# Optimization experiments

Measured on AMD Instinct MI355X. Metric: run time of the kernel, lower is better.

Reference implementation:

```python
import jax, jax.numpy as jnp
import numpy as np

B, IMG, PATCH = 32, 224, 16
D_MODEL, DEPTH = 384, 24
D_INNER, D_STATE, DT_RANK, D_CONV = 768, 16, 24, 4
L = (IMG // PATCH) ** 2  # 196 patch tokens
NCLS = 1000
EPS = 1e-5


def _layernorm(x, w, b):
    mu = x.mean(-1, keepdims=True)
    var = ((x - mu) ** 2).mean(-1, keepdims=True)
    return (x - mu) * jax.lax.rsqrt(var + EPS) * w + b


def _mamba(x, p):
    # x: [B, L, D_MODEL] -> Mamba mixer (expand=2, d_state=16, d_conv=4)
    xz = jnp.einsum('bld,ed->ble', x, p['W_in'])  # [B,L,2*di]
    xc, z = jnp.split(xz, 2, axis=-1)
    # depthwise causal conv over the sequence dim
    xt = jnp.moveaxis(xc, 1, 2)  # [B,di,L]
    xt = jnp.pad(xt, ((0, 0), (0, 0), (D_CONV - 1, 0)))
    xt = jax.lax.conv_general_dilated(xt, p['conv_w'][:, None, :], (1,), 'VALID',
                                      dimension_numbers=('NCH', 'OIH', 'NCH'),
                                      feature_group_count=D_INNER)
    xc = jax.nn.silu(jnp.moveaxis(xt, 1, 2) + p['conv_b'])  # [B,L,di]
    proj = jnp.einsum('ble,re->blr', xc, p['W_xp'])  # [B,L,dt_rank+2*ns]
    dt, Bs, Cs = jnp.split(proj, [DT_RANK, DT_RANK + D_STATE], axis=-1)
    delta = jax.nn.softplus(jnp.einsum('blr,er->ble', dt, p['W_dt']) + p['b_dt'])  # [B,L,di]
    A = -jnp.exp(p['A_log'])  # [di, ns]

    def step(h, inputs):
        # compute discretization per-step: avoids materializing [B,L,di,ns]
        d_t, B_t, C_t, u_t = inputs  # [B,di],[B,ns],[B,ns],[B,di]
        h = jnp.exp(d_t[:, :, None] * A) * h + (d_t * u_t)[:, :, None] * B_t[:, None, :]
        return h, jnp.einsum('bdn,bn->bd', h, C_t)

    h0 = jnp.zeros((x.shape[0], D_INNER, D_STATE), x.dtype)
    seq = (jnp.moveaxis(delta, 1, 0), jnp.moveaxis(Bs, 1, 0),
           jnp.moveaxis(Cs, 1, 0), jnp.moveaxis(xc, 1, 0))
    _, ys = jax.lax.scan(step, h0, seq)
    y = jnp.moveaxis(ys, 0, 1) + xc * p['D_p']
    y = y * jax.nn.silu(z)
    return jnp.einsum('ble,de->bld', y, p['W_out'])


def _forward(x, patch_w, patch_b, pos_embed, W_in, conv_w, conv_b, W_xp, W_dt,
             b_dt, A_log, D_p, W_out, ln_w, ln_b, normf_w, normf_b, head_w, head_b):
    # patch embed: conv stride 16, flatten to tokens
    h = jax.lax.conv_general_dilated(x, patch_w, (PATCH, PATCH), 'VALID',
                                     dimension_numbers=('NCHW', 'OIHW', 'NCHW'))
    h = h + patch_b[None, :, None, None]
    h = h.reshape(x.shape[0], D_MODEL, L).transpose(0, 2, 1)  # [B,L,D]
    h = h + pos_embed
    params = dict(W_in=W_in, conv_w=conv_w, conv_b=conv_b, W_xp=W_xp, W_dt=W_dt,
                  b_dt=b_dt, A_log=A_log, D_p=D_p, W_out=W_out, ln_w=ln_w, ln_b=ln_b)

    def block(carry, p):
        # Block: Add -> LN -> Mamba, carrying (hidden, residual)
        hidden, residual = carry
        residual = residual + hidden
        hidden = _mamba(_layernorm(residual, p['ln_w'], p['ln_b']), p)
        return (hidden, residual), None

    (hidden, residual), _ = jax.lax.scan(block, (h, jnp.zeros_like(h)), params)
    residual = residual + hidden
    h = _layernorm(residual, normf_w, normf_b)
    pooled = h.mean(axis=1)  # final_pool_type='mean'
    return pooled @ head_w.T + head_b


def setup_inputs():
    key = jax.random.key(0)
    ks = jax.random.split(key, 12)

    def rn(k, shape, scale=0.02):
        return jax.random.normal(k, shape, jnp.float32) * scale

    inp = {}
    inp['x'] = jax.random.normal(ks[0], (B, 3, IMG, IMG), jnp.float32)
    inp['patch_w'] = rn(ks[1], (D_MODEL, 3, PATCH, PATCH), 0.05)
    inp['patch_b'] = jnp.zeros((D_MODEL,), jnp.float32)
    inp['pos_embed'] = rn(ks[2], (1, L, D_MODEL))
    inp['W_in'] = rn(ks[3], (DEPTH, 2 * D_INNER, D_MODEL))
    inp['conv_w'] = rn(ks[4], (DEPTH, D_INNER, D_CONV), 0.1)
    inp['conv_b'] = jnp.zeros((DEPTH, D_INNER), jnp.float32)
    inp['W_xp'] = rn(ks[5], (DEPTH, DT_RANK + 2 * D_STATE, D_INNER))
    inp['W_dt'] = rn(ks[6], (DEPTH, D_INNER, DT_RANK), 0.1)
    inp['b_dt'] = jnp.full((DEPTH, D_INNER), -4.6, jnp.float32) + rn(ks[7], (DEPTH, D_INNER), 0.1)
    Ainit = jnp.tile(jnp.arange(1, D_STATE + 1, dtype=jnp.float32)[None, None, :], (DEPTH, D_INNER, 1))
    inp['A_log'] = jnp.log(Ainit)  # S4D-real init
    inp['D_p'] = jnp.ones((DEPTH, D_INNER), jnp.float32)
    inp['W_out'] = rn(ks[8], (DEPTH, D_MODEL, D_INNER))
    inp['ln_w'] = jnp.ones((DEPTH, D_MODEL), jnp.float32)
    inp['ln_b'] = jnp.zeros((DEPTH, D_MODEL), jnp.float32)
    inp['normf_w'] = jnp.ones((D_MODEL,), jnp.float32)
    inp['normf_b'] = jnp.zeros((D_MODEL,), jnp.float32)
    inp['head_w'] = rn(ks[9], (NCLS, D_MODEL))
    inp['head_b'] = jnp.zeros((NCLS,), jnp.float32)
    return inp


def reference(x, patch_w, patch_b, pos_embed, W_in, conv_w, conv_b, W_xp, W_dt,
              b_dt, A_log, D_p, W_out, ln_w, ln_b, normf_w, normf_b, head_w, head_b):
    return _forward(x, patch_w, patch_b, pos_embed, W_in, conv_w, conv_b, W_xp,
                    W_dt, b_dt, A_log, D_p, W_out, ln_w, ln_b, normf_w, normf_b,
                    head_w, head_b)
```

## Files before the change

kernel.cpp:

```cpp
#include <hip/hip_runtime.h>
#include <hip/hip_bf16.h>
#include <math.h>

#define BB      32
#define LTOK    196
#define DMODEL  384
#define DINNER  768
#define DSTATE  16
#define DTRANK  24
#define DCONV   4
#define PROJW   64
#define NTOK    (BB*LTOK)
#define NCLS    1000
#define EPS     1e-5f

typedef __attribute__((ext_vector_type(8))) short short8v;
typedef __attribute__((ext_vector_type(4))) float f32x4;

static __device__ __forceinline__ ushort f2bf(float f) {
    unsigned u = __float_as_uint(f);
    unsigned r = (u + 0x7fffu + ((u >> 16) & 1u)) >> 16;
    return (ushort)r;
}
static __device__ __forceinline__ float bf2f(ushort h) {
    return __uint_as_float(((unsigned)h) << 16);
}

__global__ void cast_bf16_kernel(const float* __restrict__ src,
                                 ushort* __restrict__ dst, int n4)
{
    int stride = gridDim.x * blockDim.x;
    for (int i = blockIdx.x * blockDim.x + threadIdx.x; i < n4; i += stride) {
        float4 v = ((const float4*)src)[i];
        ushort4 o;
        o.x = f2bf(v.x); o.y = f2bf(v.y); o.z = f2bf(v.z); o.w = f2bf(v.w);
        ((ushort4*)dst)[i] = o;
    }
}

__global__ void pad_wxp_kernel(const float* __restrict__ src, ushort* __restrict__ dst)
{
    int idx = blockIdx.x * 256 + threadIdx.x;
    if (idx >= 24 * 64 * 768) return;
    int c = idx % 768;
    int r = (idx / 768) & 63;
    int l = idx / (64 * 768);
    dst[idx] = (r < 56) ? f2bf(src[((size_t)l * 56 + r) * 768 + c]) : (ushort)0;
}

__global__ void pad_wdt_kernel(const float* __restrict__ src, ushort* __restrict__ dst)
{
    int idx = blockIdx.x * 256 + threadIdx.x;
    if (idx >= 24 * 768 * 32) return;
    int c = idx & 31;
    int r = (idx / 32) % 768;
    int l = idx / (768 * 32);
    dst[idx] = (c < 24) ? f2bf(src[((size_t)l * 768 + r) * 24 + c]) : (ushort)0;
}

template<int BM, int BN>
__global__ __launch_bounds__(256) void gemm_mfma(
    const ushort* __restrict__ A,
    const ushort* __restrict__ B,
    float* __restrict__ Cf, ushort* __restrict__ Cbf,
    int N, int K,
    const float* __restrict__ bias,
    const float* __restrict__ rowbias,
    int act, int mode)
{
    constexpr int MI = BM / 32;
    constexpr int NI = BN / 32;
    __shared__ __align__(16) ushort As[BM * 40];
    __shared__ __align__(16) ushort Bs[BN * 40];
    const int t    = threadIdx.x;
    const int lane = t & 63;
    const int wave = t >> 6;
    const int wr   = wave >> 1;
    const int wc   = wave & 1;
    const int lr   = lane & 15;
    const int lk   = lane >> 4;
    const int bm   = blockIdx.x * BM;
    const int bn   = blockIdx.y * BN;

    f32x4 acc[MI][NI];
    #pragma unroll
    for (int i = 0; i < MI; i++)
        #pragma unroll
        for (int j = 0; j < NI; j++) acc[i][j] = (f32x4){0.f, 0.f, 0.f, 0.f};

    for (int k0 = 0; k0 < K; k0 += 32) {
        #pragma unroll
        for (int i = 0; i < BM / 64; i++) {
            int c = t + i * 256;
            int row = c >> 2, kc = (c & 3) * 8;
            *(int4*)&As[row * 40 + kc] = *(const int4*)&A[(size_t)(bm + row) * K + k0 + kc];
        }
        #pragma unroll
        for (int i = 0; i < BN / 64; i++) {
            int c = t + i * 256;
            int row = c >> 2, kc = (c & 3) * 8;
            *(int4*)&Bs[row * 40 + kc] = *(const int4*)&B[(size_t)(bn + row) * K + k0 + kc];
        }
        __syncthreads();
        short8v af[MI], bfr[NI];
        #pragma unroll
        for (int mi = 0; mi < MI; mi++)
            af[mi] = *(short8v*)&As[(wr * (BM / 2) + mi * 16 + lr) * 40 + lk * 8];
        #pragma unroll
        for (int ni = 0; ni < NI; ni++)
            bfr[ni] = *(short8v*)&Bs[(wc * (BN / 2) + ni * 16 + lr) * 40 + lk * 8];
        #pragma unroll
        for (int mi = 0; mi < MI; mi++)
            #pragma unroll
            for (int ni = 0; ni < NI; ni++)
                acc[mi][ni] = __builtin_amdgcn_mfma_f32_16x16x32_bf16(
                    af[mi], bfr[ni], acc[mi][ni], 0, 0, 0);
        __syncthreads();
    }

    #pragma unroll
    for (int mi = 0; mi < MI; mi++) {
        #pragma unroll
        for (int ni = 0; ni < NI; ni++) {
            int col = bn + wc * (BN / 2) + ni * 16 + lr;
            float bv = bias ? bias[col] : 0.f;
            #pragma unroll
            for (int j = 0; j < 4; j++) {
                int row = bm + wr * (BM / 2) + mi * 16 + lk * 4 + j;
                float v = acc[mi][ni][j] + bv;
                if (rowbias) v += rowbias[(size_t)(row % LTOK) * N + col];
                if (act == 1) v = (v > 20.f) ? v : logf(1.f + __expf(v));
                if (mode == 0) {
                    Cf[(size_t)row * N + col] = v;
                } else if (mode == 1) {
                    Cbf[(size_t)row * N + col] = f2bf(v);
                } else {
                    Cf[(size_t)row * N + col] = v;
                    if (col < 32)
                        Cbf[(size_t)row * 32 + col] = (col < DTRANK) ? f2bf(v) : (ushort)0;
                }
            }
        }
    }
}

__global__ void im2col_kernel(const float* __restrict__ x, ushort* __restrict__ col)
{
    int idx = blockIdx.x * 256 + threadIdx.x;
    if (idx >= NTOK * 768) return;
    int k = idx % 768;
    int m = idx / 768;
    int b = m / LTOK, l = m % LTOK;
    int ph = l / 14, pw = l % 14;
    int c = k / 256, rr = k % 256;
    int i = rr / 16, j = rr % 16;
    col[idx] = f2bf(x[(((size_t)b * 3 + c) * 224 + ph * 16 + i) * 224 + pw * 16 + j]);
}

__global__ __launch_bounds__(64) void add_ln_kernel(
    float* __restrict__ residual, const float* __restrict__ hidden,
    const float* __restrict__ w, const float* __restrict__ b,
    float* __restrict__ xln, ushort* __restrict__ xln_bf)
{
    const int token = blockIdx.x;
    const int lane  = threadIdx.x;
    const size_t base = (size_t)token * DMODEL;
    float v[6];
    float sum = 0.f;
    #pragma unroll
    for (int i = 0; i < 6; i++) {
        int d = lane + i * 64;
        float r = residual[base + d] + hidden[base + d];
        v[i] = r;
        sum += r;
    }
    #pragma unroll
    for (int off = 32; off > 0; off >>= 1) sum += __shfl_xor(sum, off);
    float mu = sum * (1.f / DMODEL);
    float var = 0.f;
    #pragma unroll
    for (int i = 0; i < 6; i++) { float c = v[i] - mu; var += c * c; }
    #pragma unroll
    for (int off = 32; off > 0; off >>= 1) var += __shfl_xor(var, off);
    var *= (1.f / DMODEL);
    float rstd = rsqrtf(var + EPS);
    #pragma unroll
    for (int i = 0; i < 6; i++) {
        int d = lane + i * 64;
        residual[base + d] = v[i];
        float o = (v[i] - mu) * rstd * w[d] + b[d];
        xln[base + d]    = o;
        xln_bf[base + d] = f2bf(o);
    }
}

__global__ __launch_bounds__(256) void conv_silu_kernel(
    const ushort* __restrict__ xz,
    const float* __restrict__ cw,
    const float* __restrict__ cb,
    float* __restrict__ out,
    ushort* __restrict__ out_bf)
{
    int idx = blockIdx.x * 256 + threadIdx.x;
    if (idx >= NTOK * DINNER) return;
    int e = idx % DINNER;
    int m = idx / DINNER;
    int b = m / LTOK, tpos = m % LTOK;
    float4 w4 = ((const float4*)cw)[e];
    float wv[4] = {w4.x, w4.y, w4.z, w4.w};
    float acc = cb[e];
    #pragma unroll
    for (int tau = 0; tau < DCONV; tau++) {
        int l = tpos - (DCONV - 1) + tau;
        if (l >= 0)
            acc += wv[tau] * bf2f(xz[((size_t)(b * LTOK + l)) * (2 * DINNER) + e]);
    }
    float s = acc / (1.f + __expf(-acc));
    out[idx]    = s;
    out_bf[idx] = f2bf(s);
}

__global__ __launch_bounds__(64) void scan_kernel(
    const float* __restrict__ delta,
    const float* __restrict__ u,
    const float* __restrict__ proj,
    const ushort* __restrict__ xz,
    const float* __restrict__ A_log,
    const float* __restrict__ Dp,
    ushort* __restrict__ y)
{
    const int b = blockIdx.x;
    const int d = blockIdx.y * 64 + threadIdx.x;
    float Arow[DSTATE];
    #pragma unroll
    for (int n = 0; n < DSTATE; n++) Arow[n] = -__expf(A_log[(size_t)d * DSTATE + n]);
    const float ddp = Dp[d];
    float h[DSTATE];
    #pragma unroll
    for (int n = 0; n < DSTATE; n++) h[n] = 0.f;

    for (int l = 0; l < LTOK; l++) {
        const size_t row = (size_t)b * LTOK + l;
        const float dt = delta[row * DINNER + d];
        const float ut = u[row * DINNER + d];
        float Bv[DSTATE], Cv[DSTATE];
        const float4* prB = (const float4*)(proj + row * PROJW + DTRANK);
        const float4* prC = (const float4*)(proj + row * PROJW + DTRANK + DSTATE);
        #pragma unroll
        for (int q = 0; q < 4; q++) {
            float4 b4 = prB[q];
            Bv[q*4+0]=b4.x; Bv[q*4+1]=b4.y; Bv[q*4+2]=b4.z; Bv[q*4+3]=b4.w;
            float4 c4 = prC[q];
            Cv[q*4+0]=c4.x; Cv[q*4+1]=c4.y; Cv[q*4+2]=c4.z; Cv[q*4+3]=c4.w;
        }
        const float du = dt * ut;
        float acc = 0.f;
        #pragma unroll
        for (int n = 0; n < DSTATE; n++) {
            h[n] = __expf(dt * Arow[n]) * h[n] + du * Bv[n];
            acc += h[n] * Cv[n];
        }
        float zz = bf2f(xz[row * (2 * DINNER) + DINNER + d]);
        float g  = zz / (1.f + __expf(-zz));
        y[row * DINNER + d] = f2bf((acc + ut * ddp) * g);
    }
}

__global__ __launch_bounds__(256) void pool_kernel(const float* __restrict__ xln,
                                                   float* __restrict__ pooled)
{
    int idx = blockIdx.x * 256 + threadIdx.x;
    if (idx >= BB * DMODEL) return;
    int b = idx / DMODEL, d = idx % DMODEL;
    float s = 0.f;
    for (int l = 0; l < LTOK; l++) s += xln[((size_t)b * LTOK + l) * DMODEL + d];
    pooled[idx] = s * (1.f / LTOK);
}

__global__ __launch_bounds__(256) void head_kernel(const float* __restrict__ pooled,
                                                   const float* __restrict__ hw,
                                                   const float* __restrict__ hb,
                                                   float* __restrict__ out)
{
    int idx = blockIdx.x * 256 + threadIdx.x;
    if (idx >= BB * NCLS) return;
    int b = idx / NCLS, n = idx % NCLS;
    float s = hb[n];
    const float* p = pooled + (size_t)b * DMODEL;
    const float* w = hw + (size_t)n * DMODEL;
    for (int k = 0; k < DMODEL; k++) s += p[k] * w[k];
    out[idx] = s;
}

extern "C" void kernel_launch(void* const* d_in, const int* in_sizes, int n_in,
                              void* d_out, int out_size, void* d_ws, size_t ws_size,
                              hipStream_t stream)
{
    const float* x       = (const float*)d_in[0];
    const float* patch_w = (const float*)d_in[1];
    const float* patch_b = (const float*)d_in[2];
    const float* pos     = (const float*)d_in[3];
    const float* W_in    = (const float*)d_in[4];
    const float* conv_w  = (const float*)d_in[5];
    const float* conv_b  = (const float*)d_in[6];
    const float* W_xp    = (const float*)d_in[7];
    const float* W_dt    = (const float*)d_in[8];
    const float* b_dt    = (const float*)d_in[9];
    const float* A_log   = (const float*)d_in[10];
    const float* D_p     = (const float*)d_in[11];
    const float* W_out   = (const float*)d_in[12];
    const float* ln_w    = (const float*)d_in[13];
    const float* ln_b    = (const float*)d_in[14];
    const float* normf_w = (const float*)d_in[15];
    const float* normf_b = (const float*)d_in[16];
    const float* head_w  = (const float*)d_in[17];
    const float* head_b  = (const float*)d_in[18];
    float* out = (float*)d_out;

    float* wsf = (float*)d_ws;
    size_t off = 0;
    float* xcv    = wsf + off; off += (size_t)NTOK * DINNER;
    float* proj   = wsf + off; off += (size_t)NTOK * PROJW;
    float* delta  = wsf + off; off += (size_t)NTOK * DINNER;
    float* resid  = wsf + off; off += (size_t)NTOK * DMODEL;
    float* hid    = wsf + off; off += (size_t)NTOK * DMODEL;
    float* xln    = wsf + off; off += (size_t)NTOK * DMODEL;
    float* pooled = wsf + off; off += (size_t)BB * DMODEL;
    ushort* wsu = (ushort*)(wsf + off);
    size_t uoff = 0;
    ushort* Win_bf    = wsu + uoff; uoff += (size_t)24 * 1536 * DMODEL;
    ushort* Wout_bf   = wsu + uoff; uoff += (size_t)24 * DMODEL * DINNER;
    ushort* patchw_bf = wsu + uoff; uoff += (size_t)DMODEL * 768;
    ushort* Wxp_bf    = wsu + uoff; uoff += (size_t)24 * 64 * DINNER;
    ushort* Wdt_bf    = wsu + uoff; uoff += (size_t)24 * DINNER * 32;
    ushort* xln_bf    = wsu + uoff; uoff += (size_t)NTOK * DMODEL;
    ushort* xz_bf     = wsu + uoff; uoff += (size_t)NTOK * 1536;
    ushort* xcv_bf    = wsu + uoff; uoff += (size_t)NTOK * DINNER;
    ushort* dtpad_bf  = wsu + uoff; uoff += (size_t)NTOK * 32;
    ushort* y_bf      = wsu + uoff; uoff += (size_t)NTOK * DINNER;
    ushort* col_bf    = y_bf;

    cast_bf16_kernel<<<2048, 256, 0, stream>>>(W_in,    Win_bf,    24 * 1536 * DMODEL / 4);
    cast_bf16_kernel<<<2048, 256, 0, stream>>>(W_out,   Wout_bf,   24 * DMODEL * DINNER / 4);
    cast_bf16_kernel<<<256,  256, 0, stream>>>(patch_w, patchw_bf, DMODEL * 768 / 4);
    pad_wxp_kernel<<<(24 * 64 * 768 + 255) / 256, 256, 0, stream>>>(W_xp, Wxp_bf);
    pad_wdt_kernel<<<(24 * 768 * 32 + 255) / 256, 256, 0, stream>>>(W_dt, Wdt_bf);

    hipMemsetAsync(resid, 0, (size_t)NTOK * DMODEL * sizeof(float), stream);

    im2col_kernel<<<(NTOK * 768 + 255) / 256, 256, 0, stream>>>(x, col_bf);
    gemm_mfma<128,128><<<dim3(NTOK / 128, DMODEL / 128), 256, 0, stream>>>(
        col_bf, patchw_bf, hid, nullptr, DMODEL, 768, patch_b, pos, 0, 0);

    for (int l = 0; l < 24; l++) {
        add_ln_kernel<<<NTOK, 64, 0, stream>>>(resid, hid,
                                               ln_w + (size_t)l * DMODEL,
                                               ln_b + (size_t)l * DMODEL, xln, xln_bf);
        gemm_mfma<128,128><<<dim3(NTOK / 128, 1536 / 128), 256, 0, stream>>>(
            xln_bf, Win_bf + (size_t)l * 1536 * DMODEL, nullptr, xz_bf,
            1536, DMODEL, nullptr, nullptr, 0, 1);
        conv_silu_kernel<<<(NTOK * DINNER + 255) / 256, 256, 0, stream>>>(
            xz_bf, conv_w + (size_t)l * DINNER * DCONV, conv_b + (size_t)l * DINNER,
            xcv, xcv_bf);
        gemm_mfma<64,64><<<dim3(NTOK / 64, 1), 256, 0, stream>>>(
            xcv_bf, Wxp_bf + (size_t)l * 64 * DINNER, proj, dtpad_bf,
            64, DINNER, nullptr, nullptr, 0, 2);
        gemm_mfma<128,128><<<dim3(NTOK / 128, DINNER / 128), 256, 0, stream>>>(
            dtpad_bf, Wdt_bf + (size_t)l * DINNER * 32, delta, nullptr,
            DINNER, 32, b_dt + (size_t)l * DINNER, nullptr, 1, 0);
        scan_kernel<<<dim3(BB, DINNER / 64), 64, 0, stream>>>(
            delta, xcv, proj, xz_bf,
            A_log + (size_t)l * DINNER * DSTATE, D_p + (size_t)l * DINNER, y_bf);
        gemm_mfma<128,128><<<dim3(NTOK / 128, DMODEL / 128), 256, 0, stream>>>(
            y_bf, Wout_bf + (size_t)l * DMODEL * DINNER, hid, nullptr,
            DMODEL, DINNER, nullptr, nullptr, 0, 0);
    }

    add_ln_kernel<<<NTOK, 64, 0, stream>>>(resid, hid, normf_w, normf_b, xln, xln_bf);
    pool_kernel<<<(BB * DMODEL + 255) / 256, 256, 0, stream>>>(xln, pooled);
    head_kernel<<<(BB * NCLS + 255) / 256, 256, 0, stream>>>(pooled, head_w, head_b, out);
}
```

Baseline: 5.567 ms.

## Parallelize selective scan across sequence chunks with two-pass carry propagation

Replaces the sequential per-channel scan over 196 tokens with a chunked scan: 14 chunks of 14 tokens run in parallel threads. Each computes a local state from zero plus the summed delta, shares them via shared memory, then reconstructs its incoming state and recomputes outputs. This adds parallelism to a launch that previously had only 384 small 64-thread blocks, at the cost of doing the recurrence twice, an extra O(chunks) carry loop, and heavy register and shared memory use per 896-thread block.

```diff
diff --git a/kernel.cpp b/kernel.cpp
--- a/kernel.cpp
+++ b/kernel.cpp
@@ -13,6 +13,8 @@
 #define NTOK    (BB*LTOK)
 #define NCLS    1000
 #define EPS     1e-5f
+#define NCH     14
+#define CL      14
 
 typedef __attribute__((ext_vector_type(8))) short short8v;
 typedef __attribute__((ext_vector_type(4))) float f32x4;
@@ -220,7 +222,7 @@
     out_bf[idx] = f2bf(s);
 }
 
-__global__ __launch_bounds__(64) void scan_kernel(
+__global__ __launch_bounds__(896) void scan_chunked_kernel(
     const float* __restrict__ delta,
     const float* __restrict__ u,
     const float* __restrict__ proj,
@@ -229,36 +231,74 @@
     const float* __restrict__ Dp,
     ushort* __restrict__ y)
 {
-    const int b = blockIdx.x;
-    const int d = blockIdx.y * 64 + threadIdx.x;
+    __shared__ float S_l[NCH][64];
+    __shared__ float hl[NCH][DSTATE][64];
+    const int b  = blockIdx.x;
+    const int dl = threadIdx.x;
+    const int c  = threadIdx.y;
+    const int d  = blockIdx.y * 64 + dl;
+
     float Arow[DSTATE];
     #pragma unroll
     for (int n = 0; n < DSTATE; n++) Arow[n] = -__expf(A_log[(size_t)d * DSTATE + n]);
-    const float ddp = Dp[d];
+
+    const size_t row0 = (size_t)b * LTOK + c * CL;
+    float dts[CL], us[CL];
     float h[DSTATE];
     #pragma unroll
     for (int n = 0; n < DSTATE; n++) h[n] = 0.f;
-
-    for (int l = 0; l < LTOK; l++) {
-        const size_t row = (size_t)b * LTOK + l;
+    float S = 0.f;
+
+    for (int i = 0; i < CL; i++) {
+        const size_t row = row0 + i;
         const float dt = delta[row * DINNER + d];
         const float ut = u[row * DINNER + d];
-        float Bv[DSTATE], Cv[DSTATE];
+        dts[i] = dt; us[i] = ut;
+        S += dt;
+        const float du = dt * ut;
+        const float4* prB = (const float4*)(proj + row * PROJW + DTRANK);
+        #pragma unroll
+        for (int q = 0; q < 4; q++) {
+            float4 b4 = prB[q];
+            h[q*4+0] = __expf(dt * Arow[q*4+0]) * h[q*4+0] + du * b4.x;
+            h[q*4+1] = __expf(dt * Arow[q*4+1]) * h[q*4+1] + du * b4.y;
+            h[q*4+2] = __expf(dt * Arow[q*4+2]) * h[q*4+2] + du * b4.z;
+            h[q*4+3] = __expf(dt * Arow[q*4+3]) * h[q*4+3] + du * b4.w;
+        }
+    }
+    S_l[c][dl] = S;
+    #pragma unroll
+    for (int n = 0; n < DSTATE; n++) hl[c][n][dl] = h[n];
+    __syncthreads();
+
+    float hin[DSTATE];
+    #pragma unroll
+    for (int n = 0; n < DSTATE; n++) hin[n] = 0.f;
+    for (int cp = 0; cp < c; cp++) {
+        const float Sp = S_l[cp][dl];
+        #pragma unroll
+        for (int n = 0; n < DSTATE; n++)
+            hin[n] = __expf(Sp * Arow[n]) * hin[n] + hl[cp][n][dl];
+    }
+
+    const float ddp = Dp[d];
+    for (int i = 0; i < CL; i++) {
+        const size_t row = row0 + i;
+        const float dt = dts[i], ut = us[i];
+        const float du = dt * ut;
         const float4* prB = (const float4*)(proj + row * PROJW + DTRANK);
         const float4* prC = (const float4*)(proj + row * PROJW + DTRANK + DSTATE);
+        float acc = 0.f;
         #pragma unroll
         for (int q = 0; q < 4; q++) {
             float4 b4 = prB[q];
-            Bv[q*4+0]=b4.x; Bv[q*4+1]=b4.y; Bv[q*4+2]=b4.z; Bv[q*4+3]=b4.w;
             float4 c4 = prC[q];
-            Cv[q*4+0]=c4.x; Cv[q*4+1]=c4.y; Cv[q*4+2]=c4.z; Cv[q*4+3]=c4.w;
-        }
-        const float du = dt * ut;
-        float acc = 0.f;
-        #pragma unroll
-        for (int n = 0; n < DSTATE; n++) {
-            h[n] = __expf(dt * Arow[n]) * h[n] + du * Bv[n];
-            acc += h[n] * Cv[n];
+            hin[q*4+0] = __expf(dt * Arow[q*4+0]) * hin[q*4+0] + du * b4.x;
+            hin[q*4+1] = __expf(dt * Arow[q*4+1]) * hin[q*4+1] + du * b4.y;
+            hin[q*4+2] = __expf(dt * Arow[q*4+2]) * hin[q*4+2] + du * b4.z;
+            hin[q*4+3] = __expf(dt * Arow[q*4+3]) * hin[q*4+3] + du * b4.w;
+            acc += hin[q*4+0] * c4.x + hin[q*4+1] * c4.y +
+                   hin[q*4+2] * c4.z + hin[q*4+3] * c4.w;
         }
         float zz = bf2f(xz[row * (2 * DINNER) + DINNER + d]);
         float g  = zz / (1.f + __expf(-zz));
@@ -368,7 +408,7 @@
         gemm_mfma<128,128><<<dim3(NTOK / 128, DINNER / 128), 256, 0, stream>>>(
             dtpad_bf, Wdt_bf + (size_t)l * DINNER * 32, delta, nullptr,
             DINNER, 32, b_dt + (size_t)l * DINNER, nullptr, 1, 0);
-        scan_kernel<<<dim3(BB, DINNER / 64), 64, 0, stream>>>(
+        scan_chunked_kernel<<<dim3(BB, DINNER / 64), dim3(64, NCH), 0, stream>>>(
             delta, xcv, proj, xz_bf,
             A_log + (size_t)l * DINNER * DSTATE, D_p + (size_t)l * DINNER, y_bf);
         gemm_mfma<128,128><<<dim3(NTOK / 128, DMODEL / 128), 256, 0, stream>>>(
```

Result: slower. 8.976 ms (+61.2%).
